# Performance work log

Hardware: AMD Instinct MI355X
Metric: run time of the kernel (lower is better)

Reference implementation:

```python
import jax, jax.numpy as jnp
import numpy as np

RATES = (6, 12, 18, 24)  # dilation/padding per branch


def _offset_conv(x, w, b, rate):
    # mmcv ConvModule with norm_cfg=None: conv (bias=True) + ReLU
    y = jax.lax.conv_general_dilated(
        x, w, window_strides=(1, 1),
        padding=[(rate, rate), (rate, rate)],
        rhs_dilation=(rate, rate),
        dimension_numbers=('NCHW', 'OIHW', 'NCHW'))
    return jax.nn.relu(y + b[None, :, None, None])


def _deform_conv(x, offset, w, rate):
    # DCNv1: 3x3 deformable conv, stride 1, padding=dilation=rate,
    # deformable_groups=1, no bias. Zero padding outside image (bilinear).
    B, C, H, W = x.shape
    K = 9  # 3x3 kernel taps, row-major; offset channels [2k]=dy, [2k+1]=dx
    ky = (jnp.arange(K) // 3 - 1).astype(x.dtype)
    kx = (jnp.arange(K) % 3 - 1).astype(x.dtype)
    off = offset.reshape(B, K, 2, H, W)
    gy = jnp.arange(H, dtype=x.dtype)
    gx = jnp.arange(W, dtype=x.dtype)
    # sampling coords [B,K,H,W]: p0 + dilated kernel offset + learned offset
    py = gy[None, None, :, None] + ky[None, :, None, None] * rate + off[:, :, 0]
    px = gx[None, None, None, :] + kx[None, :, None, None] * rate + off[:, :, 1]
    y0 = jnp.floor(py)
    x0 = jnp.floor(px)
    wy = (py - y0)[:, None]  # [B,1,K,H,W]
    wx = (px - x0)[:, None]
    y0i = y0.astype(jnp.int32)
    x0i = x0.astype(jnp.int32)
    xf = x.reshape(B, C, H * W)

    def gather(yi, xi):
        valid = (yi >= 0) & (yi < H) & (xi >= 0) & (xi < W)
        idx = (jnp.clip(yi, 0, H - 1) * W + jnp.clip(xi, 0, W - 1)).reshape(B, K * H * W)
        v = jnp.take_along_axis(xf, idx[:, None, :], axis=2).reshape(B, C, K, H, W)
        return v * valid[:, None].astype(x.dtype)

    samp = (gather(y0i, x0i) * (1 - wy) * (1 - wx)
            + gather(y0i, x0i + 1) * (1 - wy) * wx
            + gather(y0i + 1, x0i) * wy * (1 - wx)
            + gather(y0i + 1, x0i + 1) * wy * wx)  # [B,C,K,H,W]
    return jnp.einsum('oik,bikhw->bohw', w.reshape(w.shape[0], C, K), samp)


def setup_inputs() -> dict:
    key = jax.random.key(0)
    k1, k2, k3 = jax.random.split(key, 3)
    B, C, H, W = 2, 256, 64, 64
    Cout, R = 256, len(RATES)
    x = jax.random.normal(k1, (B, C, H, W), dtype=jnp.float32)
    dweights = jax.random.normal(k2, (R, Cout, C, 3, 3), dtype=jnp.float32) * 0.02
    oweights = jax.random.normal(k3, (R, 18, C, 3, 3), dtype=jnp.float32) * 0.01
    obias = jnp.zeros((R, 18), dtype=jnp.float32)
    return {"x": x, "dweights": dweights, "oweights": oweights, "obias": obias}


def reference(x, dweights, oweights, obias):
    R = len(RATES)
    outs = []
    for i in range(R):
        j = (i - 1) % R  # source quirk: offsets[i-1] (wraps to last for i=0)
        off = _offset_conv(x, oweights[j], obias[j], RATES[j])
        outs.append(_deform_conv(x, off, dweights[i], RATES[i]))
    return jnp.concatenate(outs, axis=1)
```

## Files before the change

kernel.cpp:

```cpp
#include <hip/hip_runtime.h>
#include <hip/hip_bf16.h>

typedef __attribute__((ext_vector_type(4))) float f32x4;
typedef __attribute__((ext_vector_type(2))) _Float16 h2;
typedef __attribute__((ext_vector_type(8))) _Float16 f16x8;

#define LGKM_BARRIER() asm volatile("s_waitcnt lgkmcnt(0)\n\ts_barrier" ::: "memory")

__global__ __launch_bounds__(256) void transpose_x_hwc_f16(const float* __restrict__ x,
                                                           unsigned short* __restrict__ x16h) {
    __shared__ float s[64][65];
    int blk = blockIdx.x;
    int b = blk >> 8, ct = (blk >> 6) & 3, pt = blk & 63;
    int c0 = ct * 64, p0 = pt * 64;
    int tid = threadIdx.x;
    int tr = tid >> 6, tc = tid & 63;
#pragma unroll
    for (int i = 0; i < 16; ++i) {
        int c = i * 4 + tr;
        s[c][tc] = x[((size_t)b * 256 + c0 + c) * 4096 + p0 + tc];
    }
    __syncthreads();
#pragma unroll
    for (int i = 0; i < 16; ++i) {
        int pp = i * 4 + tr;
        _Float16 h = (_Float16)s[tc][pp];
        x16h[((size_t)b * 4096 + p0 + pp) * 256 + c0 + tc] = *(unsigned short*)&h;
    }
}

__global__ __launch_bounds__(256) void transpose_dw_f16(const float* __restrict__ dw,
                                                        unsigned short* __restrict__ wTh) {
    int idx = blockIdx.x * 256 + threadIdx.x;
    int c = idx & 255;
    int o = (idx >> 8) & 255;
    int rest = idx >> 16;
    int k = rest % 9, i = rest / 9;
    _Float16 h = (_Float16)dw[(((i << 8) + o) * 256 + c) * 9 + k];
    wTh[idx] = *(unsigned short*)&h;
}

__global__ __launch_bounds__(256) void transpose_ow_f16(const float* __restrict__ ow,
                                                        unsigned short* __restrict__ owTh) {
    int idx = blockIdx.x * 256 + threadIdx.x;
    int c = idx & 255;
    int m = (idx >> 8) & 31;
    int rk = idx >> 13;
    int k = rk % 9, r = rk / 9;
    float v = (m < 18) ? ow[((r * 18 + m) * 256 + c) * 9 + k] : 0.f;
    _Float16 h = (_Float16)v;
    owTh[idx] = *(unsigned short*)&h;
}

__global__ __launch_bounds__(512) void offset_mfma2f(const unsigned short* __restrict__ x16h,
                                                     const unsigned short* __restrict__ owTh,
                                                     const float* __restrict__ obias,
                                                     float* __restrict__ off) {
    __shared__ short    s_a[4][32][8];
    __shared__ short    s_b[4][128][8];
    __shared__ int      s_pix[9][128];
    __shared__ unsigned s_msk[9][128];

    const int blk = blockIdx.x;
    const int r = (blk & 7) >> 1, b = blk & 1;
    const int px0 = (blk >> 3) << 7;
    const int rate = 6 * (r + 1);

    const int tid = threadIdx.x;
    const int lane = tid & 63;
    const int w = tid >> 6;
    const int kg = lane >> 4, lm = lane & 15;
    const int sg = tid >> 7, spx = tid & 127;
    const int mA = (tid & 127) >> 2, kgA = tid & 3;

    const unsigned short* xbh = x16h + (size_t)b * 1048576;
    const unsigned short* wrb = owTh + (size_t)r * 9 * 32 * 256;

    for (int e = tid; e < 1152; e += 512) {
        int k = e >> 7, pl = e & 127;
        int pg = px0 + pl;
        int yy = (pg >> 6) + (k / 3 - 1) * rate;
        int xx = (pg & 63) + (k % 3 - 1) * rate;
        bool v = ((unsigned)yy < 64u) && ((unsigned)xx < 64u);
        int cy = min(max(yy, 0), 63), cx = min(max(xx, 0), 63);
        s_pix[k][pl] = cy * 64 + cx;
        s_msk[k][pl] = v ? 0xFFFFFFFFu : 0u;
    }
    __syncthreads();

    f32x4 acc0 = (f32x4)(0.f), acc1 = (f32x4)(0.f);

    uint4 a, v;
    if (tid < 128) a = *(const uint4*)(wrb + (size_t)mA * 256 + kgA * 8);
    {
        int pix = s_pix[0][spx];
        v = *(const uint4*)(xbh + (size_t)pix * 256 + sg * 8);
    }
    unsigned m = s_msk[0][spx];

    for (int t = 0; t < 72; ++t) {
        uint4 pk = make_uint4(v.x & m, v.y & m, v.z & m, v.w & m);

        LGKM_BARRIER();
        if (tid < 128) *(uint4*)&s_a[kgA][mA][0] = a;
        *(uint4*)&s_b[sg][spx][0] = pk;
        LGKM_BARRIER();

        if (t < 71) {
            int tn = t + 1, tapn = tn >> 3, c0n = (tn & 7) << 5;
            if (tid < 128)
                a = *(const uint4*)(wrb + ((size_t)tapn * 32 + mA) * 256 + c0n + kgA * 8);
            int pix = s_pix[tapn][spx];
            m = s_msk[tapn][spx];
            v = *(const uint4*)(xbh + (size_t)pix * 256 + c0n + sg * 8);
        }

        f16x8 bf  = *(const f16x8*)&s_b[kg][w * 16 + lm][0];
        f16x8 af0 = *(const f16x8*)&s_a[kg][lm][0];
        f16x8 af1 = *(const f16x8*)&s_a[kg][16 + lm][0];
        acc0 = __builtin_amdgcn_mfma_f32_16x16x32_f16(af0, bf, acc0, 0, 0, 0);
        acc1 = __builtin_amdgcn_mfma_f32_16x16x32_f16(af1, bf, acc1, 0, 0, 0);
    }

    const float* bias = obias + r * 18;
    float* ob = off + (size_t)(r * 2 + b) * 18 * 4096;
    int px = px0 + w * 16 + lm;
#pragma unroll
    for (int reg = 0; reg < 4; ++reg) {
        int mm = kg * 4 + reg;
        ob[(size_t)mm * 4096 + px] = fmaxf(acc0[reg] + bias[mm], 0.f);
        int m1 = 16 + mm;
        if (m1 < 18)
            ob[(size_t)m1 * 4096 + px] = fmaxf(acc1[reg] + bias[m1], 0.f);
    }
}

__global__ __launch_bounds__(512, 2) void deform_mfma9(const unsigned short* __restrict__ x16h,
                                                       const unsigned short* __restrict__ wTh,
                                                       const float* __restrict__ off,
                                                       float* __restrict__ out) {
    __shared__ short  s_a[256][64];
    __shared__ short  s_b[64][64];
    __shared__ int4   s_pix[9][64];
    __shared__ float4 s_wt[9][64];

    const int blk = blockIdx.x;
    const int i = (blk & 7) >> 1, b = blk & 1;
    const int px0 = (blk >> 3) << 6;
    const int r = (i + 3) & 3;
    const int rate = 6 * (i + 1);

    const int tid = threadIdx.x;
    const int lane = tid & 63;
    const int w = tid >> 6;
    const int wo = w >> 1, wp = w & 1;
    const int kg = lane >> 4, lm = lane & 15;
    const int pxS = tid >> 3, chgS = tid & 7;
    const int oA = tid >> 3, partA = tid & 7;
    const int colA = (partA * 8) ^ ((oA & 7) * 8);

    const unsigned short* xbh = x16h + (size_t)b * 1048576;
    const float* offb = off + (size_t)(r * 2 + b) * 18 * 4096;
    const unsigned short* wib = wTh + (size_t)i * 9 * 65536;

    for (int e = tid; e < 576; e += 512) {
        int k = e >> 6, pl = e & 63;
        int pg = px0 + pl;
        int yy = pg >> 6, xc = pg & 63;
        float dy = offb[(size_t)(2 * k) * 4096 + pg];
        float dx = offb[(size_t)(2 * k + 1) * 4096 + pg];
        float py = (float)(yy + (k / 3 - 1) * rate) + dy;
        float pxf = (float)(xc + (k % 3 - 1) * rate) + dx;
        float fy = floorf(py), fx = floorf(pxf);
        int y0 = (int)fy, x0 = (int)fx;
        float wy = py - fy, wx = pxf - fx;
        float vy0 = ((unsigned)y0 < 64u) ? 1.f : 0.f;
        float vy1 = ((unsigned)(y0 + 1) < 64u) ? 1.f : 0.f;
        float vx0 = ((unsigned)x0 < 64u) ? 1.f : 0.f;
        float vx1 = ((unsigned)(x0 + 1) < 64u) ? 1.f : 0.f;
        int cy0 = min(max(y0, 0), 63), cy1 = min(max(y0 + 1, 0), 63);
        int cx0 = min(max(x0, 0), 63), cx1 = min(max(x0 + 1, 0), 63);
        s_pix[k][pl] = make_int4(cy0 * 64 + cx0, cy0 * 64 + cx1,
                                 cy1 * 64 + cx0, cy1 * 64 + cx1);
        s_wt[k][pl] = make_float4(vy0 * vx0 * (1.f - wy) * (1.f - wx),
                                  vy0 * vx1 * (1.f - wy) * wx,
                                  vy1 * vx0 * wy * (1.f - wx),
                                  vy1 * vx1 * wy * wx);
    }
    __syncthreads();

    f32x4 acc[4][2];
#pragma unroll
    for (int mi = 0; mi < 4; ++mi) {
        acc[mi][0] = (f32x4)(0.f);
        acc[mi][1] = (f32x4)(0.f);
    }

    uint4 a0, a1, a2, a3, v0, v1, v2, v3;
    {
        const unsigned short* wrow = wib + partA * 8;
        a0 = *(const uint4*)(wrow + (size_t)(oA      ) * 256);
        a1 = *(const uint4*)(wrow + (size_t)(oA +  64) * 256);
        a2 = *(const uint4*)(wrow + (size_t)(oA + 128) * 256);
        a3 = *(const uint4*)(wrow + (size_t)(oA + 192) * 256);
        int4 p = s_pix[0][pxS];
        const unsigned short* xch = xbh + chgS * 8;
        v0 = *(const uint4*)(xch + ((size_t)p.x << 8));
        v1 = *(const uint4*)(xch + ((size_t)p.y << 8));
        v2 = *(const uint4*)(xch + ((size_t)p.z << 8));
        v3 = *(const uint4*)(xch + ((size_t)p.w << 8));
    }

    for (int t = 0; t < 36; ++t) {
        const int tap = t >> 2;

        uint4 pk;
        {
            float4 qwf = s_wt[tap][pxS];
            h2 qx = (h2)((_Float16)qwf.x), qy = (h2)((_Float16)qwf.y);
            h2 qz = (h2)((_Float16)qwf.z), qv = (h2)((_Float16)qwf.w);
            h2 r0 = (*(h2*)&v0.x) * qx + (*(h2*)&v1.x) * qy + (*(h2*)&v2.x) * qz + (*(h2*)&v3.x) * qv;
            h2 r1 = (*(h2*)&v0.y) * qx + (*(h2*)&v1.y) * qy + (*(h2*)&v2.y) * qz + (*(h2*)&v3.y) * qv;
            h2 r2 = (*(h2*)&v0.z) * qx + (*(h2*)&v1.z) * qy + (*(h2*)&v2.z) * qz + (*(h2*)&v3.z) * qv;
            h2 r3 = (*(h2*)&v0.w) * qx + (*(h2*)&v1.w) * qy + (*(h2*)&v2.w) * qz + (*(h2*)&v3.w) * qv;
            pk = make_uint4(*(unsigned*)&r0, *(unsigned*)&r1, *(unsigned*)&r2, *(unsigned*)&r3);
        }

        LGKM_BARRIER();
        *(uint4*)&s_a[oA      ][colA] = a0;
        *(uint4*)&s_a[oA +  64][colA] = a1;
        *(uint4*)&s_a[oA + 128][colA] = a2;
        *(uint4*)&s_a[oA + 192][colA] = a3;
        *(uint4*)&s_b[pxS][(chgS ^ (pxS & 7)) * 8] = pk;
        LGKM_BARRIER();

        if (t < 35) {
            int tn = t + 1, tapn = tn >> 2, c0n = (tn & 3) << 6;
            const unsigned short* wrow = wib + (size_t)tapn * 65536 + c0n + partA * 8;
            a0 = *(const uint4*)(wrow + (size_t)(oA      ) * 256);
            a1 = *(const uint4*)(wrow + (size_t)(oA +  64) * 256);
            a2 = *(const uint4*)(wrow + (size_t)(oA + 128) * 256);
            a3 = *(const uint4*)(wrow + (size_t)(oA + 192) * 256);
            int4 p = s_pix[tapn][pxS];
            const unsigned short* xch = xbh + c0n + chgS * 8;
            v0 = *(const uint4*)(xch + ((size_t)p.x << 8));
            v1 = *(const uint4*)(xch + ((size_t)p.y << 8));
            v2 = *(const uint4*)(xch + ((size_t)p.z << 8));
            v3 = *(const uint4*)(xch + ((size_t)p.w << 8));
        }

#pragma unroll
        for (int kf = 0; kf < 2; ++kf) {
            int oct = kf * 4 + kg;
            int bcol = (oct ^ (lm & 7)) * 8;
            f16x8 bf0 = *(const f16x8*)&s_b[wp * 32 + lm][bcol];
            f16x8 bf1 = *(const f16x8*)&s_b[wp * 32 + 16 + lm][bcol];
#pragma unroll
            for (int mi = 0; mi < 4; ++mi) {
                int o = wo * 64 + mi * 16 + lm;
                int col = (oct * 8) ^ ((o & 7) * 8);
                f16x8 af = *(const f16x8*)&s_a[o][col];
                acc[mi][0] = __builtin_amdgcn_mfma_f32_16x16x32_f16(af, bf0, acc[mi][0], 0, 0, 0);
                acc[mi][1] = __builtin_amdgcn_mfma_f32_16x16x32_f16(af, bf1, acc[mi][1], 0, 0, 0);
            }
        }
    }

    float* ob = out + ((size_t)b * 1024 + i * 256) * 4096;
#pragma unroll
    for (int mi = 0; mi < 4; ++mi) {
        int o = wo * 64 + mi * 16 + kg * 4;
#pragma unroll
        for (int ni = 0; ni < 2; ++ni) {
            int pg = px0 + wp * 32 + ni * 16 + lm;
#pragma unroll
            for (int reg = 0; reg < 4; ++reg)
                ob[(size_t)(o + reg) * 4096 + pg] = acc[mi][ni][reg];
        }
    }
}

extern "C" void kernel_launch(void* const* d_in, const int* in_sizes, int n_in,
                              void* d_out, int out_size, void* d_ws, size_t ws_size,
                              hipStream_t stream) {
    const float* x  = (const float*)d_in[0];
    const float* dw = (const float*)d_in[1];
    const float* ow = (const float*)d_in[2];
    const float* ob = (const float*)d_in[3];
    float* out = (float*)d_out;

    float* ws  = (float*)d_ws;
    float* off = ws;
    unsigned short* wTh  = (unsigned short*)(ws + 589824);
    unsigned short* owTh = wTh + 2359296;
    unsigned short* x16h = (unsigned short*)(ws + 1916928);

    transpose_x_hwc_f16<<<512, 256, 0, stream>>>(x, x16h);
    transpose_dw_f16<<<9216, 256, 0, stream>>>(dw, wTh);
    transpose_ow_f16<<<1152, 256, 0, stream>>>(ow, owTh);
    offset_mfma2f<<<256, 512, 0, stream>>>(x16h, owTh, ob, off);
    deform_mfma9<<<512, 512, 0, stream>>>(x16h, wTh, off, out);
}
```

Before: 113.4 us.

## Coalesce deform weight transpose via LDS and double K-chunk in offset conv

The deform weight transpose now loads each output channel's contiguous 2304 floats into shared memory with float4 loads and writes 9 coalesced rows. The old version did strided scalar gathers across 9216 blocks. The offset conv kernel now processes 64 input channels per barrier iteration instead of 32, which halves the loop trip count and the number of barriers, at the cost of more registers and double the LDS staging.

New measurement: 105.1 us. -7.3%, faster.

```diff
diff --git a/kernel.cpp b/kernel.cpp
--- a/kernel.cpp
+++ b/kernel.cpp
@@ -31,13 +31,20 @@
 
 __global__ __launch_bounds__(256) void transpose_dw_f16(const float* __restrict__ dw,
                                                         unsigned short* __restrict__ wTh) {
-    int idx = blockIdx.x * 256 + threadIdx.x;
-    int c = idx & 255;
-    int o = (idx >> 8) & 255;
-    int rest = idx >> 16;
-    int k = rest % 9, i = rest / 9;
-    _Float16 h = (_Float16)dw[(((i << 8) + o) * 256 + c) * 9 + k];
-    wTh[idx] = *(unsigned short*)&h;
+    __shared__ float s[2304];
+    int blk = blockIdx.x;
+    int i = blk >> 8, o = blk & 255;
+    const float* src = dw + (size_t)(i * 256 + o) * 2304;
+    int tid = threadIdx.x;
+#pragma unroll
+    for (int e = tid; e < 576; e += 256)
+        *(float4*)&s[e * 4] = *(const float4*)&src[e * 4];
+    __syncthreads();
+#pragma unroll
+    for (int k = 0; k < 9; ++k) {
+        _Float16 h = (_Float16)s[tid * 9 + k];
+        wTh[(((size_t)i * 9 + k) * 256 + o) * 256 + tid] = *(unsigned short*)&h;
+    }
 }
 
 __global__ __launch_bounds__(256) void transpose_ow_f16(const float* __restrict__ ow,
@@ -52,12 +59,12 @@
     owTh[idx] = *(unsigned short*)&h;
 }
 
-__global__ __launch_bounds__(512) void offset_mfma2f(const unsigned short* __restrict__ x16h,
+__global__ __launch_bounds__(512) void offset_mfma3f(const unsigned short* __restrict__ x16h,
                                                      const unsigned short* __restrict__ owTh,
                                                      const float* __restrict__ obias,
                                                      float* __restrict__ off) {
-    __shared__ short    s_a[4][32][8];
-    __shared__ short    s_b[4][128][8];
+    __shared__ short    s_a[8][32][8];
+    __shared__ short    s_b[8][128][8];
     __shared__ int      s_pix[9][128];
     __shared__ unsigned s_msk[9][128];
 
@@ -90,36 +97,52 @@
 
     f32x4 acc0 = (f32x4)(0.f), acc1 = (f32x4)(0.f);
 
-    uint4 a, v;
-    if (tid < 128) a = *(const uint4*)(wrb + (size_t)mA * 256 + kgA * 8);
+    uint4 a_lo, a_hi, v_lo, v_hi;
+    if (tid < 128) {
+        a_lo = *(const uint4*)(wrb + (size_t)mA * 256 + kgA * 8);
+        a_hi = *(const uint4*)(wrb + (size_t)mA * 256 + 32 + kgA * 8);
+    }
     {
         int pix = s_pix[0][spx];
-        v = *(const uint4*)(xbh + (size_t)pix * 256 + sg * 8);
+        v_lo = *(const uint4*)(xbh + (size_t)pix * 256 + sg * 8);
+        v_hi = *(const uint4*)(xbh + (size_t)pix * 256 + 32 + sg * 8);
     }
     unsigned m = s_msk[0][spx];
 
-    for (int t = 0; t < 72; ++t) {
-        uint4 pk = make_uint4(v.x & m, v.y & m, v.z & m, v.w & m);
+    for (int t = 0; t < 36; ++t) {
+        uint4 pkl = make_uint4(v_lo.x & m, v_lo.y & m, v_lo.z & m, v_lo.w & m);
+        uint4 pkh = make_uint4(v_hi.x & m, v_hi.y & m, v_hi.z & m, v_hi.w & m);
 
         LGKM_BARRIER();
-        if (tid < 128) *(uint4*)&s_a[kgA][mA][0] = a;
-        *(uint4*)&s_b[sg][spx][0] = pk;
+        if (tid < 128) {
+            *(uint4*)&s_a[kgA][mA][0]     = a_lo;
+            *(uint4*)&s_a[kgA + 4][mA][0] = a_hi;
+        }
+        *(uint4*)&s_b[sg][spx][0]     = pkl;
+        *(uint4*)&s_b[sg + 4][spx][0] = pkh;
         LGKM_BARRIER();
 
-        if (t < 71) {
-            int tn = t + 1, tapn = tn >> 3, c0n = (tn & 7) << 5;
-            if (tid < 128)
-                a = *(const uint4*)(wrb + ((size_t)tapn * 32 + mA) * 256 + c0n + kgA * 8);
+        if (t < 35) {
+            int tn = t + 1, tapn = tn >> 2, c0n = (tn & 3) << 6;
+            if (tid < 128) {
+                a_lo = *(const uint4*)(wrb + ((size_t)tapn * 32 + mA) * 256 + c0n + kgA * 8);
+                a_hi = *(const uint4*)(wrb + ((size_t)tapn * 32 + mA) * 256 + c0n + 32 + kgA * 8);
+            }
             int pix = s_pix[tapn][spx];
             m = s_msk[tapn][spx];
-            v = *(const uint4*)(xbh + (size_t)pix * 256 + c0n + sg * 8);
-        }
-
-        f16x8 bf  = *(const f16x8*)&s_b[kg][w * 16 + lm][0];
-        f16x8 af0 = *(const f16x8*)&s_a[kg][lm][0];
-        f16x8 af1 = *(const f16x8*)&s_a[kg][16 + lm][0];
-        acc0 = __builtin_amdgcn_mfma_f32_16x16x32_f16(af0, bf, acc0, 0, 0, 0);
-        acc1 = __builtin_amdgcn_mfma_f32_16x16x32_f16(af1, bf, acc1, 0, 0, 0);
+            v_lo = *(const uint4*)(xbh + (size_t)pix * 256 + c0n + sg * 8);
+            v_hi = *(const uint4*)(xbh + (size_t)pix * 256 + c0n + 32 + sg * 8);
+        }
+
+#pragma unroll
+        for (int kf = 0; kf < 2; ++kf) {
+            int oct = kf * 4 + kg;
+            f16x8 bf  = *(const f16x8*)&s_b[oct][w * 16 + lm][0];
+            f16x8 af0 = *(const f16x8*)&s_a[oct][lm][0];
+            f16x8 af1 = *(const f16x8*)&s_a[oct][16 + lm][0];
+            acc0 = __builtin_amdgcn_mfma_f32_16x16x32_f16(af0, bf, acc0, 0, 0, 0);
+            acc1 = __builtin_amdgcn_mfma_f32_16x16x32_f16(af1, bf, acc1, 0, 0, 0);
+        }
     }
 
     const float* bias = obias + r * 18;
@@ -296,8 +319,8 @@
     unsigned short* x16h = (unsigned short*)(ws + 1916928);
 
     transpose_x_hwc_f16<<<512, 256, 0, stream>>>(x, x16h);
-    transpose_dw_f16<<<9216, 256, 0, stream>>>(dw, wTh);
+    transpose_dw_f16<<<1024, 256, 0, stream>>>(dw, wTh);
     transpose_ow_f16<<<1152, 256, 0, stream>>>(ow, owTh);
-    offset_mfma2f<<<256, 512, 0, stream>>>(x16h, owTh, ob, off);
+    offset_mfma3f<<<256, 512, 0, stream>>>(x16h, owTh, ob, off);
     deform_mfma9<<<512, 512, 0, stream>>>(x16h, wTh, off, out);
 }
```
